# Performance work log

Measured on AMD Instinct MI355X. Metric: run time of the kernel, lower is better.

## Reference

```python
import jax, jax.numpy as jnp
import numpy as np

B, S, D, J, NI = 8192, 20, 300, 512, 1000
VG = 2048 + 5 * 6  # vis_dim + 5*6 = guide feature dim


def setup_inputs() -> dict:
    key = jax.random.key(0)
    ks = jax.random.split(key, 11)
    context = jax.random.normal(ks[0], (B, S, D), jnp.float32)
    embedded = jax.random.normal(ks[1], (B, S, D), jnp.float32)
    input_labels = jax.random.randint(ks[2], (B, S), 0, 10000, dtype=jnp.int64)
    # guarantee at least one valid token per row (avoid divide-by-zero renorm)
    input_labels = input_labels.at[:, 0].set(jnp.maximum(input_labels[:, 0], 1))
    guide_input = jax.random.normal(ks[3], (NI, VG), jnp.float32)
    sent_to_image_ann = jax.random.randint(ks[4], (2 * B,), 0, NI, dtype=jnp.int64)
    # parameters (PyTorch Linear: y = x @ W.T + b)
    W_sent = jax.random.normal(ks[5], (J, D), jnp.float32) * 0.02
    b_sent = jnp.zeros((J,), jnp.float32)
    W_emb = jax.random.normal(ks[6], (J, VG), jnp.float32) * 0.02
    b_emb = jnp.zeros((J,), jnp.float32)
    w_fc = jax.random.normal(ks[7], (J,), jnp.float32) * 0.02
    b_fc = jnp.zeros((), jnp.float32)
    return {"context": context, "embedded": embedded, "input_labels": input_labels,
            "guide_input": guide_input, "sent_to_image_ann": sent_to_image_ann,
            "W_sent": W_sent, "b_sent": b_sent, "W_emb": W_emb, "b_emb": b_emb,
            "w_fc": w_fc, "b_fc": b_fc}


def reference(context, embedded, input_labels, guide_input, sent_to_image_ann,
              W_sent, b_sent, W_emb, b_emb, w_fc, b_fc):
    # prefix-valid mask: loop in original breaks at first zero label
    nonzero = (input_labels != 0).astype(jnp.float32)          # (B,S)
    valid = jnp.cumprod(nonzero, axis=1)                        # (B,S)
    # per-sentence guide feature: guide_input[sent_to_image_ann[2*i]]
    fea = guide_input[sent_to_image_ann[::2]]                   # (B,VG)
    # fc_embed(guidance): guidance rows are fea (valid prefix) or 0 (else),
    # so the linear output is fea@W_emb.T+b_emb or just b_emb.
    fea_emb = fea @ W_emb.T + b_emb                             # (B,J)
    guid_emb = valid[:, :, None] * fea_emb[:, None, :] + (1.0 - valid)[:, :, None] * b_emb
    cxt_emb = jnp.einsum('bsd,jd->bsj', context, W_sent) + b_sent
    H = jnp.tanh(cxt_emb + guid_emb)                            # (B,S,J)
    scores = jnp.einsum('bsj,j->bs', H, w_fc) + b_fc            # (B,S)
    attn = jax.nn.softmax(scores, axis=1)
    attn = attn * nonzero
    attn = attn / jnp.sum(attn, axis=1, keepdims=True)
    weighted_cxt = jnp.einsum('bs,bsd->bd', attn, embedded)     # (B,D)
    return weighted_cxt
```

## Files before the change

### kernel.cpp

```cpp
#include <hip/hip_runtime.h>
#include <hip/hip_bf16.h>

#define BB 8192
#define SS 20
#define DD 300
#define JJ 512
#define NII 1000
#define VGG 2078
#define KP 328
#define RBY 656
#define BTILE 41984
#define FLP 516
#define BP1 72

typedef __attribute__((ext_vector_type(8))) short short8v;
typedef __attribute__((ext_vector_type(4))) float float4v;

__device__ __forceinline__ unsigned short bf16u(float x) {
    __hip_bfloat16 h = __float2bfloat16(x);
    return *(unsigned short*)&h;
}
__device__ __forceinline__ float bfraw2f(unsigned short u) {
    return __uint_as_float((unsigned)u << 16);
}

__global__ __launch_bounds__(256) void kc_pad_bf16(const float* __restrict__ src,
                                                   __hip_bfloat16* __restrict__ dst,
                                                   int rows, int scols, int dcols) {
    int idx = blockIdx.x * 256 + threadIdx.x;
    if (idx >= rows * dcols) return;
    int r = idx / dcols, c = idx % dcols;
    float v = (c < scols) ? src[(long)r * scols + c] : 0.f;
    dst[idx] = __float2bfloat16(v);
}

__global__ __launch_bounds__(256) void kc_prep_wsb(const float* __restrict__ W_sent,
                                                   const float* __restrict__ b_sent,
                                                   const float* __restrict__ b_emb,
                                                   __hip_bfloat16* __restrict__ dst) {
    int idx = blockIdx.x * 256 + threadIdx.x;
    if (idx >= JJ * KP) return;
    int j = idx / KP, c = idx % KP;
    float v = (c < DD) ? W_sent[(long)j * DD + c]
            : (c == DD) ? b_sent[j]
            : (c == DD + 1) ? b_emb[j] : 0.f;
    dst[idx] = __float2bfloat16(v);
}

__global__ __launch_bounds__(512) void kS_sumwf(const float* __restrict__ w_fc,
                                                float* __restrict__ out) {
    __shared__ float part[8];
    int t = threadIdx.x;
    float v = w_fc[t];
    v += __shfl_xor(v, 1);  v += __shfl_xor(v, 2);  v += __shfl_xor(v, 4);
    v += __shfl_xor(v, 8);  v += __shfl_xor(v, 16); v += __shfl_xor(v, 32);
    if ((t & 63) == 0) part[t >> 6] = v;
    __syncthreads();
    if (t == 0) {
        float s = 0.f;
#pragma unroll
        for (int i = 0; i < 8; ++i) s += part[i];
        out[0] = s;
    }
}

__global__ __launch_bounds__(256) void k0_valid(const int* __restrict__ labels,
                                                float* __restrict__ valid,
                                                float* __restrict__ nonzero) {
    int b = blockIdx.x * blockDim.x + threadIdx.x;
    if (b >= BB) return;
    float v = 1.f;
    for (int s = 0; s < SS; ++s) {
        float nz = (labels[b * SS + s] != 0) ? 1.f : 0.f;
        v *= nz;
        nonzero[b * SS + s] = nz;
        valid[b * SS + s] = v;
    }
}

__global__ __launch_bounds__(256) void k1_femb_mfma(
    const __hip_bfloat16* __restrict__ Gb,
    const __hip_bfloat16* __restrict__ Web,
    const float* __restrict__ b_emb,
    __hip_bfloat16* __restrict__ femb) {
    __shared__ __hip_bfloat16 Al[64 * BP1];
    __shared__ __hip_bfloat16 Bl[64 * BP1];
    const int t = threadIdx.x;
    const int m0 = blockIdx.x * 64;
    const int n0 = blockIdx.y * 64;
    const int lane = t & 63;
    const int w = t >> 6;
    const int wm = w >> 1, wn = w & 1;
    const int li = lane & 15, lq = lane >> 4;

    float4v acc[2][2] = {};

    for (int kt = 0; kt < 33; ++kt) {
        for (int c = t; c < 512; c += 256) {
            int rr = c >> 3, off = (c & 7) * 8;
            int gr = m0 + rr; if (gr > NII - 1) gr = NII - 1;
            *(uint4*)&Al[rr * BP1 + off] =
                *(const uint4*)(Gb + (long)gr * 2112 + kt * 64 + off);
            *(uint4*)&Bl[rr * BP1 + off] =
                *(const uint4*)(Web + (long)(n0 + rr) * 2112 + kt * 64 + off);
        }
        __syncthreads();
#pragma unroll
        for (int ks = 0; ks < 2; ++ks) {
            short8v a[2], b[2];
#pragma unroll
            for (int mt = 0; mt < 2; ++mt)
                a[mt] = *(const short8v*)&Al[(wm * 32 + mt * 16 + li) * BP1 + ks * 32 + lq * 8];
#pragma unroll
            for (int nt = 0; nt < 2; ++nt)
                b[nt] = *(const short8v*)&Bl[(wn * 32 + nt * 16 + li) * BP1 + ks * 32 + lq * 8];
#pragma unroll
            for (int mt = 0; mt < 2; ++mt)
#pragma unroll
                for (int nt = 0; nt < 2; ++nt)
                    acc[mt][nt] = __builtin_amdgcn_mfma_f32_16x16x32_bf16(
                        a[mt], b[nt], acc[mt][nt], 0, 0, 0);
        }
        __syncthreads();
    }
#pragma unroll
    for (int nt = 0; nt < 2; ++nt) {
        int col = n0 + wn * 32 + nt * 16 + li;
        float be = b_emb[col];
#pragma unroll
        for (int mt = 0; mt < 2; ++mt)
#pragma unroll
            for (int reg = 0; reg < 4; ++reg) {
                int row = wm * 32 + mt * 16 + lq * 4 + reg;
                femb[(long)(m0 + row) * JJ + col] = __float2bfloat16(acc[mt][nt][reg] + be);
            }
    }
}

__global__ __launch_bounds__(256) void k2_scores_mfma(
    const float* __restrict__ context,
    const __hip_bfloat16* __restrict__ Wsb,
    const float* __restrict__ w_fc,
    const float* __restrict__ b_fc,
    const float* __restrict__ sumwf,
    const __hip_bfloat16* __restrict__ femb,
    const int* __restrict__ ann,
    const float* __restrict__ valid,
    float* __restrict__ scores) {
    __shared__ __align__(16) char smem[41984 + 5 * FLP * 4];
    char* buf = smem;
    float* fl = (float*)(smem + 41984);

    const int t = threadIdx.x;
    const int m0 = blockIdx.x * 64;
    const int b_lo = m0 / SS;
    const int lane = t & 63;
    const int w = t >> 6;
    const int wm = w >> 1, wn = w & 1;
    const int li = lane & 15, lq = lane >> 4;

    for (int idx = t; idx < 64 * 82; idx += 256) {
        int r = idx / 82, q = idx - r * 82;
        ushort4 pk;
        if (q < 75) {
            float4 v = *(const float4*)(context + (long)(m0 + r) * DD + q * 4);
            pk.x = bf16u(v.x); pk.y = bf16u(v.y); pk.z = bf16u(v.z); pk.w = bf16u(v.w);
        } else if (q == 75) {
            pk.x = bf16u(1.f); pk.y = bf16u(1.f - valid[m0 + r]); pk.z = 0; pk.w = 0;
        } else { pk.x = pk.y = pk.z = pk.w = 0; }
        *(ushort4*)(buf + r * RBY + q * 8) = pk;
    }
    if (t < 320) {
        int i = t >> 6, ch = t & 63;
        int b = b_lo + i; if (b > BB - 1) b = BB - 1;
        int grow = ann[2 * b];
        short8v rv = *(const short8v*)(femb + (long)grow * JJ + ch * 8);
        float4 lo, hi;
        lo.x = bfraw2f((unsigned short)rv[0]); lo.y = bfraw2f((unsigned short)rv[1]);
        lo.z = bfraw2f((unsigned short)rv[2]); lo.w = bfraw2f((unsigned short)rv[3]);
        hi.x = bfraw2f((unsigned short)rv[4]); hi.y = bfraw2f((unsigned short)rv[5]);
        hi.z = bfraw2f((unsigned short)rv[6]); hi.w = bfraw2f((unsigned short)rv[7]);
        *(float4*)(fl + i * FLP + ch * 8)     = lo;
        *(float4*)(fl + i * FLP + ch * 8 + 4) = hi;
    }
    float vm[8]; int selb = 0; int br_[2];
#pragma unroll
    for (int mt = 0; mt < 2; ++mt) {
        int base = m0 + wm * 32 + mt * 16 + lq * 4;
        int br0 = base / SS - b_lo;
        br_[mt] = br0;
#pragma unroll
        for (int reg = 0; reg < 4; ++reg) {
            int m = base + reg;
            int slot = mt * 4 + reg;
            if (m / SS - b_lo != br0) selb |= (1 << slot);
            vm[slot] = valid[m];
        }
    }
    __syncthreads();

    short8v areg[2][10];
#pragma unroll
    for (int mt = 0; mt < 2; ++mt) {
        int r = wm * 32 + mt * 16 + li;
#pragma unroll
        for (int kt = 0; kt < 10; ++kt)
            areg[mt][kt] = *(const short8v*)(buf + r * RBY + kt * 64 + lq * 16);
    }

    float sp2[8] = {0.f, 0.f, 0.f, 0.f, 0.f, 0.f, 0.f, 0.f};
    const char* pB = (const char*)Wsb + (wn * 32 + li) * RBY + lq * 16;

    for (int jt = 0; jt < 8; ++jt) {
        const char* pj = pB + (long)jt * BTILE;
        float4v acc[2][2] = {};
        short8v bf0[5], bf1[5];
#pragma unroll
        for (int kt = 0; kt < 5; ++kt) {
            bf0[kt] = *(const short8v*)(pj + kt * 64);
            bf1[kt] = *(const short8v*)(pj + 16 * RBY + kt * 64);
        }
#pragma unroll
        for (int kt = 0; kt < 5; ++kt) {
            acc[0][0] = __builtin_amdgcn_mfma_f32_16x16x32_bf16(areg[0][kt], bf0[kt], acc[0][0], 0, 0, 0);
            acc[0][1] = __builtin_amdgcn_mfma_f32_16x16x32_bf16(areg[0][kt], bf1[kt], acc[0][1], 0, 0, 0);
            acc[1][0] = __builtin_amdgcn_mfma_f32_16x16x32_bf16(areg[1][kt], bf0[kt], acc[1][0], 0, 0, 0);
            acc[1][1] = __builtin_amdgcn_mfma_f32_16x16x32_bf16(areg[1][kt], bf1[kt], acc[1][1], 0, 0, 0);
        }
#pragma unroll
        for (int kt = 0; kt < 5; ++kt) {
            bf0[kt] = *(const short8v*)(pj + 320 + kt * 64);
            bf1[kt] = *(const short8v*)(pj + 16 * RBY + 320 + kt * 64);
        }
#pragma unroll
        for (int kt = 0; kt < 5; ++kt) {
            acc[0][0] = __builtin_amdgcn_mfma_f32_16x16x32_bf16(areg[0][5 + kt], bf0[kt], acc[0][0], 0, 0, 0);
            acc[0][1] = __builtin_amdgcn_mfma_f32_16x16x32_bf16(areg[0][5 + kt], bf1[kt], acc[0][1], 0, 0, 0);
            acc[1][0] = __builtin_amdgcn_mfma_f32_16x16x32_bf16(areg[1][5 + kt], bf0[kt], acc[1][0], 0, 0, 0);
            acc[1][1] = __builtin_amdgcn_mfma_f32_16x16x32_bf16(areg[1][5 + kt], bf1[kt], acc[1][1], 0, 0, 0);
        }
#pragma unroll
        for (int nt = 0; nt < 2; ++nt) {
            int col = jt * 64 + wn * 32 + nt * 16 + li;
            float wf = w_fc[col];
#pragma unroll
            for (int mt = 0; mt < 2; ++mt) {
                int br = br_[mt];
                int br1 = (br < 4) ? br + 1 : 4;
                float f0 = fl[br * FLP + col];
                float f1 = fl[br1 * FLP + col];
#pragma unroll
                for (int reg = 0; reg < 4; ++reg) {
                    int slot = mt * 4 + reg;
                    float fv = ((selb >> slot) & 1) ? f1 : f0;
                    float x = acc[mt][nt][reg] + vm[slot] * fv;
                    float e = __expf(2.f * x);
                    float r = __builtin_amdgcn_rcpf(e + 1.f);
                    sp2[slot] += wf * r;
                }
            }
        }
    }

#pragma unroll
    for (int slot = 0; slot < 8; ++slot) {
        float v = sp2[slot];
        v += __shfl_xor(v, 1); v += __shfl_xor(v, 2);
        v += __shfl_xor(v, 4); v += __shfl_xor(v, 8);
        sp2[slot] = v;
    }
    __syncthreads();
    float* red = (float*)smem;
    if (li == 0) {
#pragma unroll
        for (int mt = 0; mt < 2; ++mt)
#pragma unroll
            for (int reg = 0; reg < 4; ++reg)
                red[wn * 64 + wm * 32 + mt * 16 + lq * 4 + reg] = sp2[mt * 4 + reg];
    }
    __syncthreads();
    if (t < 64)
        scores[m0 + t] = b_fc[0] + sumwf[0] - 2.f * (red[t] + red[64 + t]);
}

__global__ __launch_bounds__(256) void k3_out(const float* __restrict__ scores,
                                              const float* __restrict__ nonzero,
                                              const float* __restrict__ embedded,
                                              float* __restrict__ out) {
    __shared__ float wgt[3][SS];
    const int b0 = blockIdx.x * 3;
    const int t = threadIdx.x;
    if (t < 3) {
        int b = b0 + t;
        if (b < BB) {
            float sc[SS], nz[SS];
            float mx = -1e30f;
            for (int s = 0; s < SS; ++s) {
                sc[s] = scores[b * SS + s];
                nz[s] = nonzero[b * SS + s];
                mx = fmaxf(mx, sc[s]);
            }
            float den = 0.f, e[SS];
            for (int s = 0; s < SS; ++s) { e[s] = nz[s] * __expf(sc[s] - mx); den += e[s]; }
            float inv = 1.f / den;
            for (int s = 0; s < SS; ++s) wgt[t][s] = e[s] * inv;
        }
    }
    __syncthreads();
    if (t < 225) {
        int r = t / 75, q = t - r * 75;
        int b = b0 + r;
        if (b < BB) {
            float4 a; a.x = a.y = a.z = a.w = 0.f;
#pragma unroll
            for (int s = 0; s < SS; ++s) {
                float4 e = *(const float4*)(embedded + ((long)b * SS + s) * DD + q * 4);
                float ww = wgt[r][s];
                a.x += ww * e.x; a.y += ww * e.y; a.z += ww * e.z; a.w += ww * e.w;
            }
            *(float4*)(out + (long)b * DD + q * 4) = a;
        }
    }
}

extern "C" void kernel_launch(void* const* d_in, const int* in_sizes, int n_in,
                              void* d_out, int out_size, void* d_ws, size_t ws_size,
                              hipStream_t stream) {
    const float* context  = (const float*)d_in[0];
    const float* embedded = (const float*)d_in[1];
    const int*   labels   = (const int*)d_in[2];
    const float* guide    = (const float*)d_in[3];
    const int*   ann      = (const int*)d_in[4];
    const float* W_sent   = (const float*)d_in[5];
    const float* b_sent   = (const float*)d_in[6];
    const float* W_emb    = (const float*)d_in[7];
    const float* b_emb    = (const float*)d_in[8];
    const float* w_fc     = (const float*)d_in[9];
    const float* b_fc     = (const float*)d_in[10];
    float* out = (float*)d_out;

    char* w = (char*)d_ws;
    __hip_bfloat16* femb = (__hip_bfloat16*)(w);
    float* valid         = (float*)(w + 1048576);
    float* nonzero       = (float*)(w + 1703936);
    float* scores        = (float*)(w + 2359296);
    __hip_bfloat16* Wsb  = (__hip_bfloat16*)(w + 3014656);
    __hip_bfloat16* Web  = (__hip_bfloat16*)(w + 3350528);
    __hip_bfloat16* Gb   = (__hip_bfloat16*)(w + 5513216);
    float* sums          = (float*)(w + 9737216);

    hipLaunchKernelGGL(kc_prep_wsb, dim3((JJ * KP + 255) / 256), dim3(256), 0, stream,
                       W_sent, b_sent, b_emb, Wsb);
    hipLaunchKernelGGL(kc_pad_bf16, dim3((JJ * 2112 + 255) / 256), dim3(256), 0, stream,
                       W_emb, Web, JJ, VGG, 2112);
    hipLaunchKernelGGL(kc_pad_bf16, dim3((NII * 2112 + 255) / 256), dim3(256), 0, stream,
                       guide, Gb, NII, VGG, 2112);
    hipLaunchKernelGGL(kS_sumwf, dim3(1), dim3(512), 0, stream, w_fc, sums);
    hipLaunchKernelGGL(k0_valid, dim3(BB / 256), dim3(256), 0, stream,
                       labels, valid, nonzero);
    hipLaunchKernelGGL(k1_femb_mfma, dim3(16, JJ / 64), dim3(256), 0, stream,
                       Gb, Web, b_emb, femb);
    hipLaunchKernelGGL(k2_scores_mfma, dim3((BB * SS) / 64), dim3(256), 0, stream,
                       context, Wsb, w_fc, b_fc, sums, femb, ann, valid, scores);
    hipLaunchKernelGGL(k3_out, dim3((BB + 2) / 3), dim3(256), 0, stream,
                       scores, nonzero, embedded, out);
}
```

Before: 282.6 us.

## Stage W_sent tiles through LDS with double-buffered async loads in score kernel

The score kernel now streams the bf16 W_sent operand into LDS in 32-column tiles using global_load_lds, double-buffered so the next tile loads while the current one runs MFMA. Previously each wave read W_sent fragments straight from global memory. w_fc is also cached in LDS, and the two bf16 padding kernels are merged into a single launch. The trade-off is a barrier on every tile iteration, twice as many j-iterations, and more LDS per block, which may lower occupancy.

Result: faster. 267.3 us (-5.4%).

```diff
diff --git a/kernel.cpp b/kernel.cpp
--- a/kernel.cpp
+++ b/kernel.cpp
@@ -9,8 +9,7 @@
 #define VGG 2078
 #define KP 328
 #define RBY 656
-#define BTILE 41984
-#define FLP 516
+#define BT2 20992
 #define BP1 72
 
 typedef __attribute__((ext_vector_type(8))) short short8v;
@@ -23,15 +22,27 @@
 __device__ __forceinline__ float bfraw2f(unsigned short u) {
     return __uint_as_float((unsigned)u << 16);
 }
-
-__global__ __launch_bounds__(256) void kc_pad_bf16(const float* __restrict__ src,
-                                                   __hip_bfloat16* __restrict__ dst,
-                                                   int rows, int scols, int dcols) {
-    int idx = blockIdx.x * 256 + threadIdx.x;
-    if (idx >= rows * dcols) return;
-    int r = idx / dcols, c = idx % dcols;
-    float v = (c < scols) ? src[(long)r * scols + c] : 0.f;
-    dst[idx] = __float2bfloat16(v);
+__device__ __forceinline__ void gload16(const void* g, void* l) {
+    __builtin_amdgcn_global_load_lds(
+        (const __attribute__((address_space(1))) unsigned int*)g,
+        (__attribute__((address_space(3))) unsigned int*)l, 16, 0, 0);
+}
+
+__global__ __launch_bounds__(256) void kc_pad2(const float* __restrict__ W_emb,
+                                               const float* __restrict__ guide,
+                                               __hip_bfloat16* __restrict__ Web,
+                                               __hip_bfloat16* __restrict__ Gb) {
+    long idx = (long)blockIdx.x * 256 + threadIdx.x;
+    if (idx >= 1512L * 2112) return;
+    int r = (int)(idx / 2112), c = (int)(idx % 2112);
+    if (r < JJ) {
+        float v = (c < VGG) ? W_emb[(long)r * VGG + c] : 0.f;
+        Web[(long)r * 2112 + c] = __float2bfloat16(v);
+    } else {
+        int g = r - JJ;
+        float v = (c < VGG) ? guide[(long)g * VGG + c] : 0.f;
+        Gb[(long)g * 2112 + c] = __float2bfloat16(v);
+    }
 }
 
 __global__ __launch_bounds__(256) void kc_prep_wsb(const float* __restrict__ W_sent,
@@ -147,9 +158,10 @@
     const int* __restrict__ ann,
     const float* __restrict__ valid,
     float* __restrict__ scores) {
-    __shared__ __align__(16) char smem[41984 + 5 * FLP * 4];
-    char* buf = smem;
-    float* fl = (float*)(smem + 41984);
+    __shared__ __align__(16) char smem[54272];
+    char* buf  = smem;
+    float* fl  = (float*)(smem + 41984);
+    float* wl  = (float*)(smem + 52224);
 
     const int t = threadIdx.x;
     const int m0 = blockIdx.x * 64;
@@ -180,9 +192,12 @@
         lo.z = bfraw2f((unsigned short)rv[2]); lo.w = bfraw2f((unsigned short)rv[3]);
         hi.x = bfraw2f((unsigned short)rv[4]); hi.y = bfraw2f((unsigned short)rv[5]);
         hi.z = bfraw2f((unsigned short)rv[6]); hi.w = bfraw2f((unsigned short)rv[7]);
-        *(float4*)(fl + i * FLP + ch * 8)     = lo;
-        *(float4*)(fl + i * FLP + ch * 8 + 4) = hi;
-    }
+        *(float4*)(fl + i * 512 + ch * 8)     = lo;
+        *(float4*)(fl + i * 512 + ch * 8 + 4) = hi;
+    }
+    wl[t] = w_fc[t];
+    wl[t + 256] = w_fc[t + 256];
+
     float vm[8]; int selb = 0; int br_[2];
 #pragma unroll
     for (int mt = 0; mt < 2; ++mt) {
@@ -207,59 +222,65 @@
         for (int kt = 0; kt < 10; ++kt)
             areg[mt][kt] = *(const short8v*)(buf + r * RBY + kt * 64 + lq * 16);
     }
-
+    __syncthreads();
+
+    {
+        const char* gB = (const char*)Wsb;
+        const int wb = w * 328;
+#pragma unroll
+        for (int i = 0; i < 5; ++i)
+            gload16(gB + (long)(wb + i * 64 + lane) * 16, buf + (wb + i * 64) * 16);
+        if (lane < 8)
+            gload16(gB + (long)(wb + 320 + lane) * 16, buf + (wb + 320) * 16);
+    }
     float sp2[8] = {0.f, 0.f, 0.f, 0.f, 0.f, 0.f, 0.f, 0.f};
-    const char* pB = (const char*)Wsb + (wn * 32 + li) * RBY + lq * 16;
-
-    for (int jt = 0; jt < 8; ++jt) {
-        const char* pj = pB + (long)jt * BTILE;
-        float4v acc[2][2] = {};
-        short8v bf0[5], bf1[5];
-#pragma unroll
-        for (int kt = 0; kt < 5; ++kt) {
-            bf0[kt] = *(const short8v*)(pj + kt * 64);
-            bf1[kt] = *(const short8v*)(pj + 16 * RBY + kt * 64);
-        }
-#pragma unroll
-        for (int kt = 0; kt < 5; ++kt) {
-            acc[0][0] = __builtin_amdgcn_mfma_f32_16x16x32_bf16(areg[0][kt], bf0[kt], acc[0][0], 0, 0, 0);
-            acc[0][1] = __builtin_amdgcn_mfma_f32_16x16x32_bf16(areg[0][kt], bf1[kt], acc[0][1], 0, 0, 0);
-            acc[1][0] = __builtin_amdgcn_mfma_f32_16x16x32_bf16(areg[1][kt], bf0[kt], acc[1][0], 0, 0, 0);
-            acc[1][1] = __builtin_amdgcn_mfma_f32_16x16x32_bf16(areg[1][kt], bf1[kt], acc[1][1], 0, 0, 0);
-        }
-#pragma unroll
-        for (int kt = 0; kt < 5; ++kt) {
-            bf0[kt] = *(const short8v*)(pj + 320 + kt * 64);
-            bf1[kt] = *(const short8v*)(pj + 16 * RBY + 320 + kt * 64);
-        }
-#pragma unroll
-        for (int kt = 0; kt < 5; ++kt) {
-            acc[0][0] = __builtin_amdgcn_mfma_f32_16x16x32_bf16(areg[0][5 + kt], bf0[kt], acc[0][0], 0, 0, 0);
-            acc[0][1] = __builtin_amdgcn_mfma_f32_16x16x32_bf16(areg[0][5 + kt], bf1[kt], acc[0][1], 0, 0, 0);
-            acc[1][0] = __builtin_amdgcn_mfma_f32_16x16x32_bf16(areg[1][5 + kt], bf0[kt], acc[1][0], 0, 0, 0);
-            acc[1][1] = __builtin_amdgcn_mfma_f32_16x16x32_bf16(areg[1][5 + kt], bf1[kt], acc[1][1], 0, 0, 0);
-        }
-#pragma unroll
-        for (int nt = 0; nt < 2; ++nt) {
-            int col = jt * 64 + wn * 32 + nt * 16 + li;
-            float wf = w_fc[col];
+    __syncthreads();
+
+    const int fragoff = (wn * 16 + li) * RBY + lq * 16;
+
+    for (int jt = 0; jt < 16; ++jt) {
+        if (jt < 15) {
+            const char* gB = (const char*)Wsb + (long)(jt + 1) * BT2;
+            char* nb = buf + ((jt + 1) & 1) * BT2;
+            const int wb = w * 328;
+#pragma unroll
+            for (int i = 0; i < 5; ++i)
+                gload16(gB + (long)(wb + i * 64 + lane) * 16, nb + (wb + i * 64) * 16);
+            if (lane < 8)
+                gload16(gB + (long)(wb + 320 + lane) * 16, nb + (wb + 320) * 16);
+        }
+
+        const char* cb = buf + (jt & 1) * BT2 + fragoff;
+        float4v acc0 = {0.f, 0.f, 0.f, 0.f}, acc1 = {0.f, 0.f, 0.f, 0.f};
+#pragma unroll
+        for (int kt = 0; kt < 10; ++kt) {
+            short8v b0 = *(const short8v*)(cb + kt * 64);
+            acc0 = __builtin_amdgcn_mfma_f32_16x16x32_bf16(areg[0][kt], b0, acc0, 0, 0, 0);
+            acc1 = __builtin_amdgcn_mfma_f32_16x16x32_bf16(areg[1][kt], b0, acc1, 0, 0, 0);
+        }
+
+        {
+            int col = jt * 32 + wn * 16 + li;
+            float wf = wl[col];
 #pragma unroll
             for (int mt = 0; mt < 2; ++mt) {
                 int br = br_[mt];
                 int br1 = (br < 4) ? br + 1 : 4;
-                float f0 = fl[br * FLP + col];
-                float f1 = fl[br1 * FLP + col];
+                float f0 = fl[br * 512 + col];
+                float f1 = fl[br1 * 512 + col];
+                float4v a = (mt == 0) ? acc0 : acc1;
 #pragma unroll
                 for (int reg = 0; reg < 4; ++reg) {
                     int slot = mt * 4 + reg;
                     float fv = ((selb >> slot) & 1) ? f1 : f0;
-                    float x = acc[mt][nt][reg] + vm[slot] * fv;
+                    float x = a[reg] + vm[slot] * fv;
                     float e = __expf(2.f * x);
                     float r = __builtin_amdgcn_rcpf(e + 1.f);
                     sp2[slot] += wf * r;
                 }
             }
         }
+        __syncthreads();
     }
 
 #pragma unroll
@@ -269,7 +290,6 @@
         v += __shfl_xor(v, 4); v += __shfl_xor(v, 8);
         sp2[slot] = v;
     }
-    __syncthreads();
     float* red = (float*)smem;
     if (li == 0) {
 #pragma unroll
@@ -351,10 +371,8 @@
 
     hipLaunchKernelGGL(kc_prep_wsb, dim3((JJ * KP + 255) / 256), dim3(256), 0, stream,
                        W_sent, b_sent, b_emb, Wsb);
-    hipLaunchKernelGGL(kc_pad_bf16, dim3((JJ * 2112 + 255) / 256), dim3(256), 0, stream,
-                       W_emb, Web, JJ, VGG, 2112);
-    hipLaunchKernelGGL(kc_pad_bf16, dim3((NII * 2112 + 255) / 256), dim3(256), 0, stream,
-                       guide, Gb, NII, VGG, 2112);
+    hipLaunchKernelGGL(kc_pad2, dim3((int)((1512L * 2112 + 255) / 256)), dim3(256), 0, stream,
+                       W_emb, guide, Web, Gb);
     hipLaunchKernelGGL(kS_sumwf, dim3(1), dim3(512), 0, stream, w_fc, sums);
     hipLaunchKernelGGL(k0_valid, dim3(BB / 256), dim3(256), 0, stream,
                        labels, valid, nonzero);
```
